# Kernel optimization log

Measured on AMD Instinct MI355X. Metric: run time of the kernel, lower is better.

## Reference

```python
import jax, jax.numpy as jnp
import numpy as np

IMAGE_SIZE = 128
NEAR = 0.1
FAR = 100.0


def setup_inputs():
    key = jax.random.key(0)
    k1, k2, k3 = jax.random.split(key, 3)
    B, N, F = 1, 1600, 2500
    S = IMAGE_SIZE
    vertices = jax.random.normal(k1, (B, N, 3), dtype=jnp.float32) * 0.5
    faces = jax.random.randint(k2, (B, F, 3), 0, N, dtype=jnp.int32)
    textures = jnp.ones((B, F, 1, 1, 1, 3), dtype=jnp.float32)
    R = jnp.broadcast_to(jnp.eye(3, dtype=jnp.float32), (B, 3, 3))
    t = jnp.array([[[0.0, 0.0, 8.0]]], dtype=jnp.float32)  # [B,1,3]
    K = jnp.array([[float(S), 0.0, S / 2.0],
                   [0.0, float(S), S / 2.0],
                   [0.0, 0.0, 1.0]], dtype=jnp.float32)
    masked_grayscale_img = jax.random.uniform(k3, (S, S), dtype=jnp.float32)
    mask_full_size = jnp.ones((S, S), dtype=jnp.float32)
    light_direction = jnp.array([1.0, -2.0, 1.0], dtype=jnp.float32)
    light_int_directional = jnp.float32(0.1)
    light_int_ambient = jnp.float32(0.1)
    return dict(vertices=vertices, faces=faces, textures=textures, R=R, t=t, K=K,
                masked_grayscale_img=masked_grayscale_img, mask_full_size=mask_full_size,
                light_direction=light_direction,
                light_int_directional=light_int_directional,
                light_int_ambient=light_int_ambient)


def _lighting_colors(vertices, faces, textures, direction, i_dir, i_amb):
    # nr.lighting with texture_size=1: per-face constant color
    fv = jax.vmap(lambda v, f: v[f])(vertices, faces)          # [B,F,3,3]
    v10 = fv[:, :, 0] - fv[:, :, 1]
    v12 = fv[:, :, 2] - fv[:, :, 1]
    n = jnp.cross(v10, v12)
    n = n / jnp.maximum(jnp.linalg.norm(n, axis=-1, keepdims=True), 1e-5)
    cos = jax.nn.relu(jnp.einsum('bfc,c->bf', n, direction))
    light = i_amb + i_dir * cos                                # [B,F]
    return textures[:, :, 0, 0, 0, :] * light[..., None]       # [B,F,3]


def _project(vertices, K, R, t, orig_size):
    # nr.projection: rigid transform, pinhole, y-flip, normalize to [-1,1]
    v = jnp.einsum('bnj,bij->bni', vertices, R) + t            # [B,N,3]
    z = v[..., 2]
    x_ = v[..., 0] / (z + 1e-9)
    y_ = v[..., 1] / (z + 1e-9)
    h = jnp.stack([x_, y_, jnp.ones_like(z)], axis=-1)
    uvw = jnp.einsum('bnj,ij->bni', h, K)
    u = uvw[..., 0]
    vv = orig_size - uvw[..., 1]
    u = 2.0 * (u - orig_size / 2.0) / orig_size
    vv = 2.0 * (vv - orig_size / 2.0) / orig_size
    return jnp.stack([u, vv, z], axis=-1)


def _rasterize_one(vproj, face, colors, S):
    # hard z-buffer rasterization, flat per-face color
    fv = vproj[face]                                            # [F,3,3]
    xy = fv[..., :2]                                            # [F,3,2]
    z = fv[..., 2]                                              # [F,3]
    ys, xs = jnp.meshgrid(jnp.arange(S), jnp.arange(S), indexing='ij')
    pxy = jnp.stack([(2.0 * xs + 1.0 - S) / S,
                     (2.0 * ys + 1.0 - S) / S], axis=-1).reshape(-1, 2)  # [P,2]

    def edge(a, b):                                             # [F,2],[F,2] -> [P,F]
        ex = b[:, 0] - a[:, 0]
        ey = b[:, 1] - a[:, 1]
        return ex[None, :] * (pxy[:, 1:2] - a[None, :, 1]) - ey[None, :] * (pxy[:, 0:1] - a[None, :, 0])

    v0, v1, v2 = xy[:, 0], xy[:, 1], xy[:, 2]
    w0 = edge(v1, v2)
    w1 = edge(v2, v0)
    w2 = edge(v0, v1)
    area = w0 + w1 + w2
    ok = jnp.abs(area) > 1e-10
    inside = (((w0 >= 0) & (w1 >= 0) & (w2 >= 0)) |
              ((w0 <= 0) & (w1 <= 0) & (w2 <= 0))) & ok
    inv_area = 1.0 / jnp.where(ok, area, 1.0)
    # perspective-correct depth: 1 / sum_k(bary_k / z_k)
    zp = 1.0 / (w0 * inv_area / z[None, :, 0]
                + w1 * inv_area / z[None, :, 1]
                + w2 * inv_area / z[None, :, 2] + 1e-12)
    inside = inside & (zp > NEAR) & (zp < FAR)
    depth = jnp.where(inside, zp, jnp.inf)                      # [P,F]
    fidx = jnp.argmin(depth, axis=1)                            # [P]
    hit = jnp.take_along_axis(inside, fidx[:, None], axis=1)[:, 0]
    pix = jnp.where(hit[:, None], colors[fidx], 0.0)            # [P,3]
    return pix.reshape(S, S, 3).transpose(2, 0, 1)              # [3,S,S]


def reference(vertices, faces, textures, R, t, K, masked_grayscale_img,
              mask_full_size, light_direction, light_int_directional,
              light_int_ambient):
    S = IMAGE_SIZE
    colors = _lighting_colors(vertices, faces, textures, light_direction,
                              light_int_directional, light_int_ambient)
    vproj = _project(vertices, K, R, t, float(S))
    image_rgb = jax.vmap(lambda vp, f, c: _rasterize_one(vp, f, c, S))(vproj, faces, colors)  # [B,3,S,S]
    image_gray = image_rgb.sum(axis=0).sum(axis=0)              # [S,S]
    image_gray = image_gray / jnp.max(image_gray)
    loss = jnp.sum((image_gray - masked_grayscale_img) ** 2) / jnp.sum(mask_full_size)
    return loss, image_rgb
```

## Files before the change

kernel.cpp:

```cpp
#include <hip/hip_runtime.h>
#include <math.h>

#define SIMG 128
#define NPIX (SIMG*SIMG)

__device__ __forceinline__ float dot3_rn(float a0,float a1,float a2,float b0,float b1,float b2){
  return __fadd_rn(__fadd_rn(__fmul_rn(a0,b0),__fmul_rn(a1,b1)),__fmul_rn(a2,b2));
}

__global__ void __launch_bounds__(256) k_raster_face(
    const float* __restrict__ verts, const int* __restrict__ faces,
    const float* __restrict__ Rm, const float* __restrict__ tv,
    const float* __restrict__ Km,
    unsigned long long* __restrict__ zbuf, int F)
{
  int f = (int)((blockIdx.x*blockDim.x + threadIdx.x) >> 6);
  if (f >= F) return;
  int lane = threadIdx.x & 63;

  float uu[3], vv2[3], zz[3];
  #pragma unroll
  for (int k=0;k<3;k++){
    int vi = faces[3*f+k];
    float X = verts[3*vi+0], Y = verts[3*vi+1], Z = verts[3*vi+2];
    float cx = __fadd_rn(dot3_rn(X,Y,Z, Rm[0],Rm[1],Rm[2]), tv[0]);
    float cy = __fadd_rn(dot3_rn(X,Y,Z, Rm[3],Rm[4],Rm[5]), tv[1]);
    float cz = __fadd_rn(dot3_rn(X,Y,Z, Rm[6],Rm[7],Rm[8]), tv[2]);
    float zd = __fadd_rn(cz, 1e-9f);
    float x_ = __fdiv_rn(cx, zd);
    float y_ = __fdiv_rn(cy, zd);
    float ur = __fadd_rn(__fadd_rn(__fmul_rn(x_,Km[0]),__fmul_rn(y_,Km[1])), Km[2]);
    float vr = __fadd_rn(__fadd_rn(__fmul_rn(x_,Km[3]),__fmul_rn(y_,Km[4])), Km[5]);
    float vflip = __fsub_rn(128.0f, vr);
    uu[k]  = __fdiv_rn(__fmul_rn(2.0f, __fsub_rn(ur,   64.0f)), 128.0f);
    vv2[k] = __fdiv_rn(__fmul_rn(2.0f, __fsub_rn(vflip,64.0f)), 128.0f);
    zz[k]  = cz;
  }
  float x0=uu[0], y0=vv2[0], x1=uu[1], y1=vv2[1], x2=uu[2], y2=vv2[2];
  float z0=zz[0], z1=zz[1], z2=zz[2];
  float e0x=__fsub_rn(x2,x1), e0y=__fsub_rn(y2,y1);
  float e1x=__fsub_rn(x0,x2), e1y=__fsub_rn(y0,y2);
  float e2x=__fsub_rn(x1,x0), e2y=__fsub_rn(y1,y0);
  float bxmin = fminf(fminf(x0,x1),x2) - 1e-4f;
  float bxmax = fmaxf(fmaxf(x0,x1),x2) + 1e-4f;
  float bymin = fminf(fminf(y0,y1),y2) - 1e-4f;
  float bymax = fmaxf(fmaxf(y0,y1),y2) + 1e-4f;

  int x0p = (int)ceilf(__fmaf_rn(64.0f, bxmin, 63.5f)) - 1;
  int x1p = (int)floorf(__fmaf_rn(64.0f, bxmax, 63.5f)) + 1;
  int y0p = (int)ceilf(__fmaf_rn(64.0f, bymin, 63.5f)) - 1;
  int y1p = (int)floorf(__fmaf_rn(64.0f, bymax, 63.5f)) + 1;
  x0p = max(x0p, 0); y0p = max(y0p, 0);
  x1p = min(x1p, SIMG-1); y1p = min(y1p, SIMG-1);
  int W = x1p - x0p + 1, H = y1p - y0p + 1;
  if (W <= 0 || H <= 0) return;
  int shift = (W <= 1) ? 0 : (32 - __clz(W - 1));
  int W2 = 1 << shift;
  int total = W2 * H;

  for (int i = lane; i < total; i += 64) {
    int xx = x0p + (i & (W2 - 1));
    int yy = y0p + (i >> shift);
    if (xx > x1p) continue;
    float px = (float)(2*xx + 1 - SIMG) / 128.0f;
    float py = (float)(2*yy + 1 - SIMG) / 128.0f;
    float w0 = __fsub_rn(__fmul_rn(e0x,__fsub_rn(py,y1)), __fmul_rn(e0y,__fsub_rn(px,x1)));
    float w1 = __fsub_rn(__fmul_rn(e1x,__fsub_rn(py,y2)), __fmul_rn(e1y,__fsub_rn(px,x2)));
    float w2 = __fsub_rn(__fmul_rn(e2x,__fsub_rn(py,y0)), __fmul_rn(e2y,__fsub_rn(px,x0)));
    float area = __fadd_rn(__fadd_rn(w0,w1),w2);
    bool sgn = (w0>=0.0f && w1>=0.0f && w2>=0.0f) || (w0<=0.0f && w1<=0.0f && w2<=0.0f);
    bool okf = fabsf(area) > 1e-10f;
    if (sgn && okf) {
      float inv = __fdiv_rn(1.0f, area);
      float q0 = __fdiv_rn(__fmul_rn(w0,inv), z0);
      float q1 = __fdiv_rn(__fmul_rn(w1,inv), z1);
      float q2 = __fdiv_rn(__fmul_rn(w2,inv), z2);
      float den = __fadd_rn(__fadd_rn(__fadd_rn(q0,q1),q2), 1e-12f);
      float zp = __fdiv_rn(1.0f, den);
      if (zp > 0.1f && zp < 100.0f) {
        unsigned long long pack =
            ((unsigned long long)(unsigned int)__float_as_int(zp) << 32) |
            (unsigned int)f;
        atomicMin(&zbuf[yy*SIMG + xx], pack);
      }
    }
  }
}

__global__ void __launch_bounds__(256) k_resolve_loss(
    const unsigned long long* __restrict__ zbuf,
    const float* __restrict__ verts, const int* __restrict__ faces,
    const float* __restrict__ tex,
    const float* __restrict__ ldir, const float* __restrict__ idir,
    const float* __restrict__ iamb,
    const float* __restrict__ mimg, const float* __restrict__ mask,
    float* __restrict__ out_rgb, float* __restrict__ gray,
    int* __restrict__ counter, int* __restrict__ gmax_i,
    float* __restrict__ out)
{
  int pix = blockIdx.x*blockDim.x + threadIdx.x;
  unsigned long long v = zbuf[pix];
  bool hit = (unsigned int)(v >> 32) < 0x7f800000u;
  float c0=0.0f, c1=0.0f, c2=0.0f;
  if (hit) {
    int w = (int)(v & 0xffffffffu);
    int i0 = faces[3*w+0], i1 = faces[3*w+1], i2 = faces[3*w+2];
    float p0x=verts[3*i0+0], p0y=verts[3*i0+1], p0z=verts[3*i0+2];
    float p1x=verts[3*i1+0], p1y=verts[3*i1+1], p1z=verts[3*i1+2];
    float p2x=verts[3*i2+0], p2y=verts[3*i2+1], p2z=verts[3*i2+2];
    float ax=__fsub_rn(p0x,p1x), ay=__fsub_rn(p0y,p1y), az=__fsub_rn(p0z,p1z);
    float bx=__fsub_rn(p2x,p1x), by=__fsub_rn(p2y,p1y), bz=__fsub_rn(p2z,p1z);
    float nx=__fsub_rn(__fmul_rn(ay,bz),__fmul_rn(az,by));
    float ny=__fsub_rn(__fmul_rn(az,bx),__fmul_rn(ax,bz));
    float nz=__fsub_rn(__fmul_rn(ax,by),__fmul_rn(ay,bx));
    float nn=__fsqrt_rn(dot3_rn(nx,ny,nz,nx,ny,nz));
    nn = fmaxf(nn, 1e-5f);
    nx=__fdiv_rn(nx,nn); ny=__fdiv_rn(ny,nn); nz=__fdiv_rn(nz,nn);
    float cosv = fmaxf(0.0f, dot3_rn(nx,ny,nz, ldir[0],ldir[1],ldir[2]));
    float light = __fadd_rn(iamb[0], __fmul_rn(idir[0], cosv));
    c0 = __fmul_rn(tex[3*w+0], light);
    c1 = __fmul_rn(tex[3*w+1], light);
    c2 = __fmul_rn(tex[3*w+2], light);
  }
  out_rgb[pix]          = c0;
  out_rgb[NPIX + pix]   = c1;
  out_rgb[2*NPIX + pix] = c2;
  float g = __fadd_rn(__fadd_rn(c0,c1),c2);
  __hip_atomic_store(&gray[pix], g, __ATOMIC_RELAXED, __HIP_MEMORY_SCOPE_AGENT);

  float m = g;
  #pragma unroll
  for (int off = 32; off > 0; off >>= 1) m = fmaxf(m, __shfl_down(m, off, 64));
  __shared__ float sm[4];
  if ((threadIdx.x & 63) == 0) sm[threadIdx.x >> 6] = m;
  __syncthreads();
  if (threadIdx.x == 0) {
    m = fmaxf(fmaxf(sm[0],sm[1]), fmaxf(sm[2],sm[3]));
    atomicMax(gmax_i, __float_as_int(m));
  }

  __shared__ int is_last;
  __threadfence();
  if (threadIdx.x == 0) {
    int p = atomicAdd(counter, 1);
    is_last = (p == (int)gridDim.x - 1);
  }
  __syncthreads();
  if (!is_last) return;
  __threadfence();

  float mx = __int_as_float(__hip_atomic_load(gmax_i, __ATOMIC_RELAXED, __HIP_MEMORY_SCOPE_AGENT));
  float ssum = 0.0f, msum = 0.0f;
  for (int j = 0; j < NPIX/256; ++j) {
    int p2 = j*256 + threadIdx.x;
    float gv = __hip_atomic_load(&gray[p2], __ATOMIC_RELAXED, __HIP_MEMORY_SCOPE_AGENT);
    float gg = __fdiv_rn(gv, mx);
    float d  = __fsub_rn(gg, mimg[p2]);
    ssum = __fadd_rn(ssum, __fmul_rn(d,d));
    msum = __fadd_rn(msum, mask[p2]);
  }
  #pragma unroll
  for (int off = 32; off > 0; off >>= 1) {
    ssum += __shfl_down(ssum, off, 64);
    msum += __shfl_down(msum, off, 64);
  }
  __shared__ float s1[4], s2[4];
  if ((threadIdx.x & 63) == 0) { s1[threadIdx.x>>6] = ssum; s2[threadIdx.x>>6] = msum; }
  __syncthreads();
  if (threadIdx.x == 0) {
    ssum = ((s1[0]+s1[1])+(s1[2]+s1[3]));
    msum = ((s2[0]+s2[1])+(s2[2]+s2[3]));
    out[0] = __fdiv_rn(ssum, msum);
  }
}

extern "C" void kernel_launch(void* const* d_in, const int* in_sizes, int n_in,
                              void* d_out, int out_size, void* d_ws, size_t ws_size,
                              hipStream_t stream)
{
  const float* verts = (const float*)d_in[0];
  const int*   faces = (const int*)  d_in[1];
  const float* tex   = (const float*)d_in[2];
  const float* Rm    = (const float*)d_in[3];
  const float* tv    = (const float*)d_in[4];
  const float* Km    = (const float*)d_in[5];
  const float* mimg  = (const float*)d_in[6];
  const float* mask  = (const float*)d_in[7];
  const float* ldir  = (const float*)d_in[8];
  const float* idir  = (const float*)d_in[9];
  const float* iamb  = (const float*)d_in[10];
  int F = in_sizes[1] / 3;

  unsigned long long* zbuf = (unsigned long long*)d_ws;
  float* gray    = (float*)(zbuf + NPIX);
  int*   gmax_i  = (int*)(gray + NPIX);
  int*   counter = gmax_i + 1;
  float* out     = (float*)d_out;

  hipMemsetAsync(zbuf, 0xFF, (size_t)NPIX*sizeof(unsigned long long), stream);
  hipMemsetAsync(gmax_i, 0, 2*sizeof(int), stream);

  hipLaunchKernelGGL(k_raster_face, dim3((F + 3)/4), dim3(256), 0, stream,
                     verts, faces, Rm, tv, Km, zbuf, F);
  hipLaunchKernelGGL(k_resolve_loss, dim3(64), dim3(256), 0, stream,
                     zbuf, verts, faces, tex, ldir, idir, iamb, mimg, mask,
                     out + 1, gray, counter, gmax_i, out);
}
```

Before: 109.6 us.

## Fuse raster and resolve into persistent kernel with grid barrier and split faces

Merges the rasterization and resolve/loss kernels into one persistent kernel of 1024 blocks. Blocks synchronise through a global atomic barrier, and the first 64 blocks then do the resolve. Each face is split into 8 wave-sized sub-items that stride over its bounding box, which spreads the work of large faces. A single memset to 0xFF now initialises the z-buffer and all counters, with the barrier and counter targets set to match the wrapped starting value. This removes one kernel launch and one memset. In exchange, every sub-item repeats the vertex projection, and the spin barrier only works if all 1024 blocks are resident at the same time.

```diff
diff --git a/kernel.cpp b/kernel.cpp
--- a/kernel.cpp
+++ b/kernel.cpp
@@ -3,103 +3,119 @@
 
 #define SIMG 128
 #define NPIX (SIMG*SIMG)
+#define SPLIT 8
+#define GRID 1024
 
 __device__ __forceinline__ float dot3_rn(float a0,float a1,float a2,float b0,float b1,float b2){
   return __fadd_rn(__fadd_rn(__fmul_rn(a0,b0),__fmul_rn(a1,b1)),__fmul_rn(a2,b2));
 }
 
-__global__ void __launch_bounds__(256) k_raster_face(
+__global__ void __launch_bounds__(256, 4) k_fused(
     const float* __restrict__ verts, const int* __restrict__ faces,
     const float* __restrict__ Rm, const float* __restrict__ tv,
     const float* __restrict__ Km,
-    unsigned long long* __restrict__ zbuf, int F)
-{
-  int f = (int)((blockIdx.x*blockDim.x + threadIdx.x) >> 6);
-  if (f >= F) return;
-  int lane = threadIdx.x & 63;
-
-  float uu[3], vv2[3], zz[3];
-  #pragma unroll
-  for (int k=0;k<3;k++){
-    int vi = faces[3*f+k];
-    float X = verts[3*vi+0], Y = verts[3*vi+1], Z = verts[3*vi+2];
-    float cx = __fadd_rn(dot3_rn(X,Y,Z, Rm[0],Rm[1],Rm[2]), tv[0]);
-    float cy = __fadd_rn(dot3_rn(X,Y,Z, Rm[3],Rm[4],Rm[5]), tv[1]);
-    float cz = __fadd_rn(dot3_rn(X,Y,Z, Rm[6],Rm[7],Rm[8]), tv[2]);
-    float zd = __fadd_rn(cz, 1e-9f);
-    float x_ = __fdiv_rn(cx, zd);
-    float y_ = __fdiv_rn(cy, zd);
-    float ur = __fadd_rn(__fadd_rn(__fmul_rn(x_,Km[0]),__fmul_rn(y_,Km[1])), Km[2]);
-    float vr = __fadd_rn(__fadd_rn(__fmul_rn(x_,Km[3]),__fmul_rn(y_,Km[4])), Km[5]);
-    float vflip = __fsub_rn(128.0f, vr);
-    uu[k]  = __fdiv_rn(__fmul_rn(2.0f, __fsub_rn(ur,   64.0f)), 128.0f);
-    vv2[k] = __fdiv_rn(__fmul_rn(2.0f, __fsub_rn(vflip,64.0f)), 128.0f);
-    zz[k]  = cz;
-  }
-  float x0=uu[0], y0=vv2[0], x1=uu[1], y1=vv2[1], x2=uu[2], y2=vv2[2];
-  float z0=zz[0], z1=zz[1], z2=zz[2];
-  float e0x=__fsub_rn(x2,x1), e0y=__fsub_rn(y2,y1);
-  float e1x=__fsub_rn(x0,x2), e1y=__fsub_rn(y0,y2);
-  float e2x=__fsub_rn(x1,x0), e2y=__fsub_rn(y1,y0);
-  float bxmin = fminf(fminf(x0,x1),x2) - 1e-4f;
-  float bxmax = fmaxf(fmaxf(x0,x1),x2) + 1e-4f;
-  float bymin = fminf(fminf(y0,y1),y2) - 1e-4f;
-  float bymax = fmaxf(fmaxf(y0,y1),y2) + 1e-4f;
-
-  int x0p = (int)ceilf(__fmaf_rn(64.0f, bxmin, 63.5f)) - 1;
-  int x1p = (int)floorf(__fmaf_rn(64.0f, bxmax, 63.5f)) + 1;
-  int y0p = (int)ceilf(__fmaf_rn(64.0f, bymin, 63.5f)) - 1;
-  int y1p = (int)floorf(__fmaf_rn(64.0f, bymax, 63.5f)) + 1;
-  x0p = max(x0p, 0); y0p = max(y0p, 0);
-  x1p = min(x1p, SIMG-1); y1p = min(y1p, SIMG-1);
-  int W = x1p - x0p + 1, H = y1p - y0p + 1;
-  if (W <= 0 || H <= 0) return;
-  int shift = (W <= 1) ? 0 : (32 - __clz(W - 1));
-  int W2 = 1 << shift;
-  int total = W2 * H;
-
-  for (int i = lane; i < total; i += 64) {
-    int xx = x0p + (i & (W2 - 1));
-    int yy = y0p + (i >> shift);
-    if (xx > x1p) continue;
-    float px = (float)(2*xx + 1 - SIMG) / 128.0f;
-    float py = (float)(2*yy + 1 - SIMG) / 128.0f;
-    float w0 = __fsub_rn(__fmul_rn(e0x,__fsub_rn(py,y1)), __fmul_rn(e0y,__fsub_rn(px,x1)));
-    float w1 = __fsub_rn(__fmul_rn(e1x,__fsub_rn(py,y2)), __fmul_rn(e1y,__fsub_rn(px,x2)));
-    float w2 = __fsub_rn(__fmul_rn(e2x,__fsub_rn(py,y0)), __fmul_rn(e2y,__fsub_rn(px,x0)));
-    float area = __fadd_rn(__fadd_rn(w0,w1),w2);
-    bool sgn = (w0>=0.0f && w1>=0.0f && w2>=0.0f) || (w0<=0.0f && w1<=0.0f && w2<=0.0f);
-    bool okf = fabsf(area) > 1e-10f;
-    if (sgn && okf) {
-      float inv = __fdiv_rn(1.0f, area);
-      float q0 = __fdiv_rn(__fmul_rn(w0,inv), z0);
-      float q1 = __fdiv_rn(__fmul_rn(w1,inv), z1);
-      float q2 = __fdiv_rn(__fmul_rn(w2,inv), z2);
-      float den = __fadd_rn(__fadd_rn(__fadd_rn(q0,q1),q2), 1e-12f);
-      float zp = __fdiv_rn(1.0f, den);
-      if (zp > 0.1f && zp < 100.0f) {
-        unsigned long long pack =
-            ((unsigned long long)(unsigned int)__float_as_int(zp) << 32) |
-            (unsigned int)f;
-        atomicMin(&zbuf[yy*SIMG + xx], pack);
-      }
-    }
-  }
-}
-
-__global__ void __launch_bounds__(256) k_resolve_loss(
-    const unsigned long long* __restrict__ zbuf,
-    const float* __restrict__ verts, const int* __restrict__ faces,
     const float* __restrict__ tex,
     const float* __restrict__ ldir, const float* __restrict__ idir,
     const float* __restrict__ iamb,
     const float* __restrict__ mimg, const float* __restrict__ mask,
-    float* __restrict__ out_rgb, float* __restrict__ gray,
-    int* __restrict__ counter, int* __restrict__ gmax_i,
-    float* __restrict__ out)
+    unsigned long long* zbuf,
+    unsigned int* bar, unsigned int* lossctr, int* gmax_i,
+    float* gray, float* out_rgb, float* out, int F)
 {
-  int pix = blockIdx.x*blockDim.x + threadIdx.x;
-  unsigned long long v = zbuf[pix];
+  int lane   = threadIdx.x & 63;
+  int wv     = (int)((blockIdx.x*blockDim.x + threadIdx.x) >> 6);
+  int nwaves = (int)((gridDim.x*blockDim.x) >> 6);
+  int nitems = F * SPLIT;
+
+  for (int item = wv; item < nitems; item += nwaves) {
+    int f   = item >> 3;
+    int sub = item & 7;
+
+    float uu[3], vv2[3], zz[3];
+    #pragma unroll
+    for (int k=0;k<3;k++){
+      int vi = faces[3*f+k];
+      float X = verts[3*vi+0], Y = verts[3*vi+1], Z = verts[3*vi+2];
+      float cx = __fadd_rn(dot3_rn(X,Y,Z, Rm[0],Rm[1],Rm[2]), tv[0]);
+      float cy = __fadd_rn(dot3_rn(X,Y,Z, Rm[3],Rm[4],Rm[5]), tv[1]);
+      float cz = __fadd_rn(dot3_rn(X,Y,Z, Rm[6],Rm[7],Rm[8]), tv[2]);
+      float zd = __fadd_rn(cz, 1e-9f);
+      float x_ = __fdiv_rn(cx, zd);
+      float y_ = __fdiv_rn(cy, zd);
+      float ur = __fadd_rn(__fadd_rn(__fmul_rn(x_,Km[0]),__fmul_rn(y_,Km[1])), Km[2]);
+      float vr = __fadd_rn(__fadd_rn(__fmul_rn(x_,Km[3]),__fmul_rn(y_,Km[4])), Km[5]);
+      float vflip = __fsub_rn(128.0f, vr);
+      uu[k]  = __fdiv_rn(__fmul_rn(2.0f, __fsub_rn(ur,   64.0f)), 128.0f);
+      vv2[k] = __fdiv_rn(__fmul_rn(2.0f, __fsub_rn(vflip,64.0f)), 128.0f);
+      zz[k]  = cz;
+    }
+    float x0=uu[0], y0=vv2[0], x1=uu[1], y1=vv2[1], x2=uu[2], y2=vv2[2];
+    float z0=zz[0], z1=zz[1], z2=zz[2];
+    float e0x=__fsub_rn(x2,x1), e0y=__fsub_rn(y2,y1);
+    float e1x=__fsub_rn(x0,x2), e1y=__fsub_rn(y0,y2);
+    float e2x=__fsub_rn(x1,x0), e2y=__fsub_rn(y1,y0);
+    float bxmin = fminf(fminf(x0,x1),x2) - 1e-4f;
+    float bxmax = fmaxf(fmaxf(x0,x1),x2) + 1e-4f;
+    float bymin = fminf(fminf(y0,y1),y2) - 1e-4f;
+    float bymax = fmaxf(fmaxf(y0,y1),y2) + 1e-4f;
+
+    int x0p = (int)ceilf(__fmaf_rn(64.0f, bxmin, 63.5f)) - 1;
+    int x1p = (int)floorf(__fmaf_rn(64.0f, bxmax, 63.5f)) + 1;
+    int y0p = (int)ceilf(__fmaf_rn(64.0f, bymin, 63.5f)) - 1;
+    int y1p = (int)floorf(__fmaf_rn(64.0f, bymax, 63.5f)) + 1;
+    x0p = max(x0p, 0); y0p = max(y0p, 0);
+    x1p = min(x1p, SIMG-1); y1p = min(y1p, SIMG-1);
+    int W = x1p - x0p + 1, H = y1p - y0p + 1;
+    if (W <= 0 || H <= 0) continue;
+    int shift = (W <= 1) ? 0 : (32 - __clz(W - 1));
+    int W2 = 1 << shift;
+    int total = W2 * H;
+
+    for (int i = sub*64 + lane; i < total; i += SPLIT*64) {
+      int xx = x0p + (i & (W2 - 1));
+      int yy = y0p + (i >> shift);
+      if (xx > x1p) continue;
+      float px = (float)(2*xx + 1 - SIMG) / 128.0f;
+      float py = (float)(2*yy + 1 - SIMG) / 128.0f;
+      float w0 = __fsub_rn(__fmul_rn(e0x,__fsub_rn(py,y1)), __fmul_rn(e0y,__fsub_rn(px,x1)));
+      float w1 = __fsub_rn(__fmul_rn(e1x,__fsub_rn(py,y2)), __fmul_rn(e1y,__fsub_rn(px,x2)));
+      float w2 = __fsub_rn(__fmul_rn(e2x,__fsub_rn(py,y0)), __fmul_rn(e2y,__fsub_rn(px,x0)));
+      float area = __fadd_rn(__fadd_rn(w0,w1),w2);
+      bool sgn = (w0>=0.0f && w1>=0.0f && w2>=0.0f) || (w0<=0.0f && w1<=0.0f && w2<=0.0f);
+      bool okf = fabsf(area) > 1e-10f;
+      if (sgn && okf) {
+        float inv = __fdiv_rn(1.0f, area);
+        float q0 = __fdiv_rn(__fmul_rn(w0,inv), z0);
+        float q1 = __fdiv_rn(__fmul_rn(w1,inv), z1);
+        float q2 = __fdiv_rn(__fmul_rn(w2,inv), z2);
+        float den = __fadd_rn(__fadd_rn(__fadd_rn(q0,q1),q2), 1e-12f);
+        float zp = __fdiv_rn(1.0f, den);
+        if (zp > 0.1f && zp < 100.0f) {
+          unsigned long long pack =
+              ((unsigned long long)(unsigned int)__float_as_int(zp) << 32) |
+              (unsigned int)f;
+          atomicMin(&zbuf[yy*SIMG + xx], pack);
+        }
+      }
+    }
+  }
+
+  __threadfence();
+  __syncthreads();
+  if (threadIdx.x == 0) {
+    __hip_atomic_fetch_add(bar, 1u, __ATOMIC_ACQ_REL, __HIP_MEMORY_SCOPE_AGENT);
+    unsigned int target = gridDim.x - 1u;
+    while (__hip_atomic_load(bar, __ATOMIC_RELAXED, __HIP_MEMORY_SCOPE_AGENT) != target)
+      __builtin_amdgcn_s_sleep(1);
+  }
+  __syncthreads();
+  __threadfence();
+
+  if (blockIdx.x >= 64) return;
+
+  int pix = (int)(blockIdx.x*blockDim.x + threadIdx.x);
+  unsigned long long v = __hip_atomic_load(&zbuf[pix], __ATOMIC_RELAXED,
+                                           __HIP_MEMORY_SCOPE_AGENT);
   bool hit = (unsigned int)(v >> 32) < 0x7f800000u;
   float c0=0.0f, c1=0.0f, c2=0.0f;
   if (hit) {
@@ -142,17 +158,19 @@
   __shared__ int is_last;
   __threadfence();
   if (threadIdx.x == 0) {
-    int p = atomicAdd(counter, 1);
-    is_last = (p == (int)gridDim.x - 1);
+    unsigned int p = __hip_atomic_fetch_add(lossctr, 1u, __ATOMIC_ACQ_REL,
+                                            __HIP_MEMORY_SCOPE_AGENT);
+    is_last = (p == 62u);
   }
   __syncthreads();
   if (!is_last) return;
   __threadfence();
 
-  float mx = __int_as_float(__hip_atomic_load(gmax_i, __ATOMIC_RELAXED, __HIP_MEMORY_SCOPE_AGENT));
+  float mx = __int_as_float(__hip_atomic_load(gmax_i, __ATOMIC_RELAXED,
+                                              __HIP_MEMORY_SCOPE_AGENT));
   float ssum = 0.0f, msum = 0.0f;
   for (int j = 0; j < NPIX/256; ++j) {
-    int p2 = j*256 + threadIdx.x;
+    int p2 = j*256 + (int)threadIdx.x;
     float gv = __hip_atomic_load(&gray[p2], __ATOMIC_RELAXED, __HIP_MEMORY_SCOPE_AGENT);
     float gg = __fdiv_rn(gv, mx);
     float d  = __fsub_rn(gg, mimg[p2]);
@@ -192,17 +210,16 @@
   int F = in_sizes[1] / 3;
 
   unsigned long long* zbuf = (unsigned long long*)d_ws;
-  float* gray    = (float*)(zbuf + NPIX);
-  int*   gmax_i  = (int*)(gray + NPIX);
-  int*   counter = gmax_i + 1;
-  float* out     = (float*)d_out;
-
-  hipMemsetAsync(zbuf, 0xFF, (size_t)NPIX*sizeof(unsigned long long), stream);
-  hipMemsetAsync(gmax_i, 0, 2*sizeof(int), stream);
-
-  hipLaunchKernelGGL(k_raster_face, dim3((F + 3)/4), dim3(256), 0, stream,
-                     verts, faces, Rm, tv, Km, zbuf, F);
-  hipLaunchKernelGGL(k_resolve_loss, dim3(64), dim3(256), 0, stream,
-                     zbuf, verts, faces, tex, ldir, idir, iamb, mimg, mask,
-                     out + 1, gray, counter, gmax_i, out);
+  unsigned char* ctrl = (unsigned char*)(zbuf + NPIX);
+  unsigned int* bar     = (unsigned int*)(ctrl + 0);
+  unsigned int* lossctr = (unsigned int*)(ctrl + 4);
+  int*          gmax_i  = (int*)        (ctrl + 8);
+  float*        gray    = (float*)      (ctrl + 64);
+  float*        out     = (float*)d_out;
+
+  hipMemsetAsync(zbuf, 0xFF, (size_t)NPIX*sizeof(unsigned long long) + 64, stream);
+
+  hipLaunchKernelGGL(k_fused, dim3(GRID), dim3(256), 0, stream,
+                     verts, faces, Rm, tv, Km, tex, ldir, idir, iamb, mimg, mask,
+                     zbuf, bar, lossctr, gmax_i, gray, out + 1, out, F);
 }
```

Result: slower. 313.4 us (+186.0%).
